# Optimization experiments

Hardware: AMD Instinct MI355X
Metric: run time of the kernel (lower is better)

Reference implementation:

```python
import jax, jax.numpy as jnp
import numpy as np
from math import erf, pi, sqrt, exp

D = 2048
TARGET_BITS = 2.5
N_HIGH = 1024  # round(D * frac)
N_LOW = D - N_HIGH
HIGH_MSE_BITS = 2  # ceil(2.5) - 1
LOW_MSE_BITS = 1   # floor(2.5) - 1


def _phi(x):
    return np.exp(-0.5 * x * x) / np.sqrt(2.0 * np.pi)


def _Phi(x):
    return 0.5 * (1.0 + np.vectorize(erf)(x / np.sqrt(2.0)))


def lloyd_max_centroids(bits: int) -> np.ndarray:
    """Lloyd-Max optimal scalar quantizer centroids for N(0,1), 2**bits levels."""
    L = 2 ** bits
    c = np.linspace(-2.0, 2.0, L)
    for _ in range(200):
        b = 0.5 * (c[:-1] + c[1:])                      # decision boundaries
        edges = np.concatenate([[-1e9], b, [1e9]])
        lo, hi = edges[:-1], edges[1:]
        mass = _Phi(hi) - _Phi(lo)
        c = (_phi(lo) - _phi(hi)) / np.maximum(mass, 1e-12)  # conditional mean
    return c.astype(np.float32)


def generate_rotation_matrix(d: int, seed: int) -> np.ndarray:
    rng = np.random.default_rng(seed)
    A = rng.standard_normal((d, d)).astype(np.float64)
    Q, R = np.linalg.qr(A)
    Q = Q * np.sign(np.diag(R))[None, :]
    return Q.astype(np.float32)


def setup_inputs() -> dict:
    key = jax.random.key(0)
    kq, kk = jax.random.split(key)
    queries = jax.random.normal(kq, (1024, D), dtype=jnp.float32)
    keys = jax.random.normal(kk, (4096, D), dtype=jnp.float32)
    Pi = jnp.asarray(generate_rotation_matrix(D, seed=42 + 2000))
    high_centroids = jnp.asarray(lloyd_max_centroids(HIGH_MSE_BITS))  # (4,)
    low_centroids = jnp.asarray(lloyd_max_centroids(LOW_MSE_BITS))    # (2,)
    rng = np.random.default_rng(42)
    S_high = jnp.asarray(rng.standard_normal((N_HIGH, N_HIGH)).astype(np.float32))
    rng2 = np.random.default_rng(42 + 1000)
    S_low = jnp.asarray(rng2.standard_normal((N_LOW, N_LOW)).astype(np.float32))
    return {"queries": queries, "keys": keys, "Pi": Pi,
            "high_centroids": high_centroids, "low_centroids": low_centroids,
            "S_high": S_high, "S_low": S_low}


def _quantize_group(y, centroids, S):
    # nearest-centroid scalar quantization per channel
    idx = jnp.argmin(jnp.abs(y[..., None] - centroids), axis=-1)  # (bk, n_ch)
    y_mse = centroids[idx]
    residual = y - y_mse
    residual_norm = jnp.linalg.norm(residual, axis=-1)            # (bk,)
    signs = jnp.sign(residual @ S.T)                              # (bk, m)
    return y_mse, signs, residual_norm


def _ip_group(q_ch, y_mse, signs, residual_norm, S):
    m = S.shape[0]
    term1 = q_ch @ y_mse.T                                        # (bq, bk)
    # QJL estimator: <q, r> ~ sqrt(pi/2)/m * ||r|| * <S q, sign(S r)>
    term2 = (jnp.sqrt(jnp.float32(pi / 2)) / m) * ((q_ch @ S.T) @ signs.T) * residual_norm[None, :]
    return term1 + term2


def reference(queries, keys, Pi, high_centroids, low_centroids, S_high, S_low):
    # ---- quantize keys ----
    vec_norm = jnp.linalg.norm(keys, axis=-1)                     # (bk,)
    k_n = keys / (vec_norm[:, None] + 1e-8)
    y = k_n @ Pi.T
    yh, yl = y[:, :N_HIGH], y[:, N_HIGH:]
    kmse_h, sg_h, rn_h = _quantize_group(yh, high_centroids, S_high)
    kmse_l, sg_l, rn_l = _quantize_group(yl, low_centroids, S_low)
    # ---- inner product estimate ----
    q_rot = queries @ Pi.T
    qh, ql = q_rot[:, :N_HIGH], q_rot[:, N_HIGH:]
    ip = _ip_group(qh, kmse_h, sg_h, rn_h, S_high) + _ip_group(ql, kmse_l, sg_l, rn_l, S_low)
    return ip * vec_norm[None, :]                                 # (bq, bk)
```

## Files before the change

### kernel.cpp

```cpp
#include <hip/hip_runtime.h>
#include <math.h>

#ifndef M_PI
#define M_PI 3.14159265358979323846
#endif

typedef __attribute__((ext_vector_type(8))) __bf16 bf16x8;
typedef __attribute__((ext_vector_type(4))) float f32x4;
typedef __attribute__((ext_vector_type(2))) float f32x2;
typedef __attribute__((ext_vector_type(8))) unsigned short ushort8;
typedef __attribute__((ext_vector_type(4))) unsigned short ushort4v;

__device__ __forceinline__ unsigned short f2bf(float x) {
    unsigned int u = __float_as_uint(x);
    unsigned int r = (u + 0x7FFFu + ((u >> 16) & 1u)) >> 16;
    return (unsigned short)r;
}

#define PKFMA_L(d, a, b) \
    asm("v_pk_fma_f32 %0, %1, %2, %0 op_sel:[0,0,0] op_sel_hi:[0,1,1]" \
        : "+v"(d) : "v"(a), "v"(b))
#define PKFMA_H(d, a, b) \
    asm("v_pk_fma_f32 %0, %1, %2, %0 op_sel:[1,0,0] op_sel_hi:[1,1,1]" \
        : "+v"(d) : "v"(a), "v"(b))

__global__ __launch_bounds__(256)
void norm_np_k(const float* __restrict__ keys,
               float* __restrict__ den,
               float* __restrict__ vnorm)
{
#pragma clang fp contract(off)
    const int tid = threadIdx.x;
    const int row_l = tid >> 4;
    const int blk = tid & 15;
    const int row = blockIdx.x * 16 + row_l;
    const float* a = keys + (size_t)row * 2048 + blk * 128;

    float r0 = a[0]*a[0], r1 = a[1]*a[1], r2 = a[2]*a[2], r3 = a[3]*a[3];
    float r4 = a[4]*a[4], r5 = a[5]*a[5], r6 = a[6]*a[6], r7 = a[7]*a[7];
    for (int i = 8; i < 128; i += 8) {
        r0 += a[i+0]*a[i+0]; r1 += a[i+1]*a[i+1];
        r2 += a[i+2]*a[i+2]; r3 += a[i+3]*a[i+3];
        r4 += a[i+4]*a[i+4]; r5 += a[i+5]*a[i+5];
        r6 += a[i+6]*a[i+6]; r7 += a[i+7]*a[i+7];
    }
    float bsum = ((r0 + r1) + (r2 + r3)) + ((r4 + r5) + (r6 + r7));

    __shared__ float bs[16][16];
    bs[row_l][blk] = bsum;
    __syncthreads();
    if (blk == 0) {
        const float* b = bs[row_l];
        float q0 = ((b[0] + b[1]) + (b[2] + b[3])) + ((b[4] + b[5]) + (b[6] + b[7]));
        float q1 = ((b[8] + b[9]) + (b[10] + b[11])) + ((b[12] + b[13]) + (b[14] + b[15]));
        float s = q0 + q1;
        float n = (float)sqrt((double)s);
        den[row] = n + 1e-8f;
        vnorm[row] = n;
    }
}

__global__ __launch_bounds__(256)
void kn_k(const float* __restrict__ keys,
          const float* __restrict__ den,
          float* __restrict__ kn)
{
#pragma clang fp contract(off)
    const int idx = (blockIdx.x * 256 + threadIdx.x) * 8;
    const int row = idx >> 11;
    const float d = den[row];
    float4 v0 = *(const float4*)(keys + idx);
    float4 v1 = *(const float4*)(keys + idx + 4);
    v0.x /= d; v0.y /= d; v0.z /= d; v0.w /= d;
    v1.x /= d; v1.y /= d; v1.z /= d; v1.w /= d;
    *(float4*)(kn + idx) = v0;
    *(float4*)(kn + idx + 4) = v1;
}

__global__ __launch_bounds__(256)
void f2bf_k(const float* __restrict__ in, unsigned short* __restrict__ out)
{
    const int i = (blockIdx.x * 256 + threadIdx.x) * 8;
    float4 v0 = *(const float4*)(in + i);
    float4 v1 = *(const float4*)(in + i + 4);
    ushort8 o;
    o[0] = f2bf(v0.x); o[1] = f2bf(v0.y); o[2] = f2bf(v0.z); o[3] = f2bf(v0.w);
    o[4] = f2bf(v1.x); o[5] = f2bf(v1.y); o[6] = f2bf(v1.z); o[7] = f2bf(v1.w);
    *(ushort8*)(out + i) = o;
}

template <int EPI>
__global__ __launch_bounds__(256, 2)
void gemm_dec_k(const float* __restrict__ A, int lda, int a_zoff,
                const float* __restrict__ B0, const float* __restrict__ B1,
                int ldb,
                float* __restrict__ Cf, unsigned short* __restrict__ Cb,
                int c_zoff, int ldc, int K,
                const float* __restrict__ rv0, const float* __restrict__ rv1)
{
#pragma clang fp contract(off)
    __shared__ float Bs[2][32][132];

    const int z = blockIdx.z;
    const float* Ap = A + (size_t)z * a_zoff;
    const float* Bp = z ? B1 : B0;
    const float* rvp = z ? rv1 : rv0;
    unsigned short* Cbp = (EPI == 1) ? (Cb + (size_t)z * c_zoff) : nullptr;

    const int tid = threadIdx.x;
    const int tr4 = (tid >> 4) * 4;
    const int tc4 = (tid & 15) * 4;
    const int row0 = blockIdx.y * 128;
    const int col0 = blockIdx.x * 128;
    const int sc  = tid >> 1;
    const int skb = (tid & 1) * 16;

    const float* gb = Bp + (size_t)(col0 + sc) * ldb + skb;

    const float* garow[8];
    #pragma unroll
    for (int i = 0; i < 4; ++i) {
        garow[i]     = Ap + (size_t)(row0 + tr4 + i) * lda;
        garow[4 + i] = Ap + (size_t)(row0 + 64 + tr4 + i) * lda;
    }

    f32x2 acc[8][4] = {};
    f32x2 agA[16], agB[16];
    float sb[16];

#define ALOAD(dst, koff) do { \
    _Pragma("unroll") \
    for (int r = 0; r < 8; ++r) \
        *(float4*)&dst[2 * r] = *(const float4*)(garow[r] + (koff)); \
} while (0)

#define BLOADG(koff) do { \
    *(float4*)(sb)      = *(const float4*)(gb + (koff)); \
    *(float4*)(sb + 4)  = *(const float4*)(gb + (koff) + 4); \
    *(float4*)(sb + 8)  = *(const float4*)(gb + (koff) + 8); \
    *(float4*)(sb + 12) = *(const float4*)(gb + (koff) + 12); \
} while (0)

#define BSTORE(buf) do { \
    _Pragma("unroll") \
    for (int u = 0; u < 16; ++u) Bs[buf][skb + u][sc] = sb[u]; \
} while (0)

    BLOADG(0);
    BSTORE(0);
    ALOAD(agA, 0);
    __syncthreads();
    int cur = 0;

    for (int k0 = 0; k0 < K; k0 += 32) {
        const bool moreP = (k0 + 32 < K);
        if (moreP) BLOADG(k0 + 32);

        #pragma unroll
        for (int g = 0; g < 8; ++g) {
            const int nko = k0 + (g + 1) * 4;
            if ((g & 1) == 0) { if (nko < K) ALOAD(agB, nko); }
            else              { if (nko < K) ALOAD(agA, nko); }
            const f32x2* acur = (g & 1) ? agB : agA;

            #pragma unroll
            for (int j = 0; j < 4; ++j) {
                const int kk = g * 4 + j;
                float4 vb0 = *(const float4*)&Bs[cur][kk][tc4];
                float4 vb1 = *(const float4*)&Bs[cur][kk][tc4 + 64];
                f32x2 fb[4];
                fb[0] = (f32x2){vb0.x, vb0.y}; fb[1] = (f32x2){vb0.z, vb0.w};
                fb[2] = (f32x2){vb1.x, vb1.y}; fb[3] = (f32x2){vb1.z, vb1.w};
                #pragma unroll
                for (int r = 0; r < 8; ++r) {
                    const f32x2 ap = acur[2 * r + (j >> 1)];
                    #pragma unroll
                    for (int q = 0; q < 4; ++q) {
                        if (j & 1) { PKFMA_H(acc[r][q], ap, fb[q]); }
                        else       { PKFMA_L(acc[r][q], ap, fb[q]); }
                    }
                }
            }
        }

        if (moreP) BSTORE(cur ^ 1);
        __syncthreads();
        cur ^= 1;
    }

    #pragma unroll
    for (int r = 0; r < 8; ++r) {
        const int row = row0 + ((r < 4) ? (tr4 + r) : (64 + tr4 + r - 4));
        if (EPI == 0) {
            float4 lo4 = {acc[r][0].x, acc[r][0].y, acc[r][1].x, acc[r][1].y};
            float4 hi4 = {acc[r][2].x, acc[r][2].y, acc[r][3].x, acc[r][3].y};
            *(float4*)&Cf[(size_t)row * ldc + col0 + tc4]      = lo4;
            *(float4*)&Cf[(size_t)row * ldc + col0 + 64 + tc4] = hi4;
        } else {
            const float s = rvp[row];
            float v[8] = {acc[r][0].x, acc[r][0].y, acc[r][1].x, acc[r][1].y,
                          acc[r][2].x, acc[r][2].y, acc[r][3].x, acc[r][3].y};
            ushort4v o0, o1;
            #pragma unroll
            for (int j = 0; j < 4; ++j) {
                const float t0 = v[j];
                o0[j] = f2bf((t0 > 0.0f) ? s : ((t0 < 0.0f) ? -s : 0.0f));
                const float t1 = v[4 + j];
                o1[j] = f2bf((t1 > 0.0f) ? s : ((t1 < 0.0f) ? -s : 0.0f));
            }
            *(ushort4v*)&Cbp[(size_t)row * ldc + col0 + tc4]      = o0;
            *(ushort4v*)&Cbp[(size_t)row * ldc + col0 + 64 + tc4] = o1;
        }
    }
#undef ALOAD
#undef BLOADG
#undef BSTORE
}

__global__ __launch_bounds__(256)
void quant_k(float* __restrict__ Y,
             unsigned short* __restrict__ Bmse,
             const float* __restrict__ ch,
             const float* __restrict__ cl,
             float* __restrict__ sc_h,
             float* __restrict__ sc_l,
             double coefd)
{
#pragma clang fp contract(off)
    const int row = blockIdx.x;
    const int tid = threadIdx.x;
    const int c0 = tid * 8;
    const float h0 = ch[0], h1 = ch[1], h2 = ch[2], h3 = ch[3];
    const float l0 = cl[0], l1 = cl[1];

    float y[8], res[8];
    ushort8 cb;
    *(float4*)(y)     = *(const float4*)(Y + (size_t)row * 2048 + c0);
    *(float4*)(y + 4) = *(const float4*)(Y + (size_t)row * 2048 + c0 + 4);

    const bool high = (tid < 128);
    float ss = 0.0f;
    #pragma unroll
    for (int j = 0; j < 8; ++j) {
        const float v = y[j];
        float cbest;
        if (high) {
            cbest = h0;
            float bd = fabsf(v - h0), dd;
            dd = fabsf(v - h1); if (dd < bd) { bd = dd; cbest = h1; }
            dd = fabsf(v - h2); if (dd < bd) { bd = dd; cbest = h2; }
            dd = fabsf(v - h3); if (dd < bd) { bd = dd; cbest = h3; }
        } else {
            cbest = (fabsf(v - l1) < fabsf(v - l0)) ? l1 : l0;
        }
        res[j] = v - cbest;
        cb[j] = f2bf(cbest);
        ss += res[j] * res[j];
    }
    *(float4*)(Y + (size_t)row * 2048 + c0)     = *(float4*)(res);
    *(float4*)(Y + (size_t)row * 2048 + c0 + 4) = *(float4*)(res + 4);
    *(ushort8*)(Bmse + (size_t)row * 4096 + c0) = cb;

    __shared__ float sm[256];
    sm[tid] = ss;
    __syncthreads();
    for (int o = 64; o > 0; o >>= 1) {
        if ((tid & 127) < o) sm[tid] += sm[tid + o];
        __syncthreads();
    }
    if (tid == 0)   sc_h[row] = (float)(coefd * sqrt((double)sm[0]));
    if (tid == 128) sc_l[row] = (float)(coefd * sqrt((double)sm[128]));
}

template <int EPI>
__global__ __launch_bounds__(256)
void gemm_mfma_k(const unsigned short* __restrict__ A, int lda, int a_zoff,
                 const unsigned short* __restrict__ B0,
                 const unsigned short* __restrict__ B1, int ldb,
                 float* __restrict__ Cf, unsigned short* __restrict__ Cb,
                 int c_zoff, int ldc, int K,
                 const float* __restrict__ colscale)
{
    __shared__ unsigned short As[128][40];
    __shared__ unsigned short Bs[128][40];

    const int z = blockIdx.z;
    const unsigned short* Ap = A + (size_t)z * a_zoff;
    const unsigned short* Bp = z ? B1 : B0;
    unsigned short* Cbp = (EPI == 2) ? (Cb + (size_t)z * c_zoff) : nullptr;

    const int tid = threadIdx.x;
    const int lane = tid & 63;
    const int wid = tid >> 6;
    const int wm = wid >> 1;
    const int wn = wid & 1;
    const int row0 = blockIdx.y * 128;
    const int col0 = blockIdx.x * 128;
    const int sr = tid >> 1;
    const int sk = (tid & 1) * 16;
    const int frow = lane & 15;
    const int fk = (lane >> 4) * 8;

    const unsigned short* ga = Ap + (size_t)(row0 + sr) * lda + sk;
    const unsigned short* gb = Bp + (size_t)(col0 + sr) * ldb + sk;

    f32x4 acc[4][4] = {};

    for (int k0 = 0; k0 < K; k0 += 32) {
        ushort8 a0 = *(const ushort8*)(ga + k0);
        ushort8 a1 = *(const ushort8*)(ga + k0 + 8);
        ushort8 b0 = *(const ushort8*)(gb + k0);
        ushort8 b1 = *(const ushort8*)(gb + k0 + 8);
        __syncthreads();
        *(ushort8*)&As[sr][sk]     = a0;
        *(ushort8*)&As[sr][sk + 8] = a1;
        *(ushort8*)&Bs[sr][sk]     = b0;
        *(ushort8*)&Bs[sr][sk + 8] = b1;
        __syncthreads();

        bf16x8 af[4], bfr[4];
        #pragma unroll
        for (int mi = 0; mi < 4; ++mi)
            af[mi] = *(const bf16x8*)&As[wm * 64 + mi * 16 + frow][fk];
        #pragma unroll
        for (int ni = 0; ni < 4; ++ni)
            bfr[ni] = *(const bf16x8*)&Bs[wn * 64 + ni * 16 + frow][fk];
        #pragma unroll
        for (int mi = 0; mi < 4; ++mi)
            #pragma unroll
            for (int ni = 0; ni < 4; ++ni)
                acc[mi][ni] = __builtin_amdgcn_mfma_f32_16x16x32_bf16(
                    af[mi], bfr[ni], acc[mi][ni], 0, 0, 0);
    }

    const int drow = (lane >> 4) * 4;
    const int dcol = lane & 15;
    #pragma unroll
    for (int mi = 0; mi < 4; ++mi) {
        #pragma unroll
        for (int ni = 0; ni < 4; ++ni) {
            const int c = col0 + wn * 64 + ni * 16 + dcol;
            const float cs = (EPI == 1) ? colscale[c] : 0.0f;
            #pragma unroll
            for (int rg = 0; rg < 4; ++rg) {
                const int r = row0 + wm * 64 + mi * 16 + drow + rg;
                const float v = acc[mi][ni][rg];
                if (EPI == 1) Cf[(size_t)r * ldc + c] = v * cs;
                else          Cbp[(size_t)r * ldc + c] = f2bf(v);
            }
        }
    }
}

extern "C" void kernel_launch(void* const* d_in, const int* in_sizes, int n_in,
                              void* d_out, int out_size, void* d_ws, size_t ws_size,
                              hipStream_t stream)
{
    const float* queries = (const float*)d_in[0];
    const float* keys    = (const float*)d_in[1];
    const float* Pi      = (const float*)d_in[2];
    const float* ch      = (const float*)d_in[3];
    const float* cl      = (const float*)d_in[4];
    const float* S_high  = (const float*)d_in[5];
    const float* S_low   = (const float*)d_in[6];
    float* out = (float*)d_out;

    char* ws = (char*)d_ws;
    float*          kn    = (float*)(ws);
    float*          Y     = (float*)(ws + ((size_t)32 << 20));
    unsigned short* Bbig  = (unsigned short*)(ws + ((size_t)64 << 20));
    unsigned short* Abig  = (unsigned short*)(ws + ((size_t)96 << 20));
    unsigned short* Qb    = (unsigned short*)(ws + ((size_t)104 << 20));
    unsigned short* Pib   = (unsigned short*)(ws + ((size_t)108 << 20));
    unsigned short* Sbh   = (unsigned short*)(ws + ((size_t)116 << 20));
    unsigned short* Sbl   = (unsigned short*)(ws + ((size_t)118 << 20));
    float*          den   = (float*)(ws + ((size_t)120 << 20));
    float*          vnorm = (float*)(ws + ((size_t)120 << 20) + 16384);
    float*          sc_h  = (float*)(ws + ((size_t)120 << 20) + 32768);
    float*          sc_l  = (float*)(ws + ((size_t)120 << 20) + 49152);

    const double coefd = sqrt(M_PI / 2.0) / 1024.0;

    norm_np_k<<<256, 256, 0, stream>>>(keys, den, vnorm);

    kn_k<<<4096, 256, 0, stream>>>(keys, den, kn);

    f2bf_k<<<1024, 256, 0, stream>>>(queries, Qb);
    f2bf_k<<<2048, 256, 0, stream>>>(Pi, Pib);
    f2bf_k<<<512, 256, 0, stream>>>(S_high, Sbh);
    f2bf_k<<<512, 256, 0, stream>>>(S_low, Sbl);

    gemm_dec_k<0><<<dim3(16, 32, 1), 256, 0, stream>>>(
        kn, 2048, 0, Pi, Pi, 2048, Y, nullptr, 0, 2048, 2048, nullptr, nullptr);

    quant_k<<<4096, 256, 0, stream>>>(Y, Bbig, ch, cl, sc_h, sc_l, coefd);

    gemm_dec_k<1><<<dim3(8, 32, 2), 256, 0, stream>>>(
        Y, 2048, 1024, S_high, S_low, 1024,
        nullptr, Bbig + 2048, 1024, 4096, 1024, sc_h, sc_l);

    gemm_mfma_k<2><<<dim3(16, 8, 1), 256, 0, stream>>>(
        Qb, 2048, 0, Pib, Pib, 2048, nullptr, Abig, 0, 4096, 2048, nullptr);
    gemm_mfma_k<2><<<dim3(8, 8, 2), 256, 0, stream>>>(
        Abig, 4096, 1024, Sbh, Sbl, 1024, nullptr, Abig + 2048, 1024, 4096, 1024, nullptr);

    gemm_mfma_k<1><<<dim3(32, 8, 1), 256, 0, stream>>>(
        Abig, 4096, 0, Bbig, Bbig, 4096, out, nullptr, 0, 4096, 4096, vnorm);
}
```

Measured before the change: 864.2 us.

## Stage A tile through LDS and enlarge fp32 GEMM tile to 256 rows

```diff
diff --git a/kernel.cpp b/kernel.cpp
--- a/kernel.cpp
+++ b/kernel.cpp
@@ -99,7 +99,8 @@
                 const float* __restrict__ rv0, const float* __restrict__ rv1)
 {
 #pragma clang fp contract(off)
-    __shared__ float Bs[2][32][132];
+    __shared__ float As[2][256][21];
+    __shared__ float Bs[2][16][132];
 
     const int z = blockIdx.z;
     const float* Ap = A + (size_t)z * a_zoff;
@@ -108,89 +109,89 @@
     unsigned short* Cbp = (EPI == 1) ? (Cb + (size_t)z * c_zoff) : nullptr;
 
     const int tid = threadIdx.x;
-    const int tr4 = (tid >> 4) * 4;
+    const int tr = tid >> 4;
     const int tc4 = (tid & 15) * 4;
-    const int row0 = blockIdx.y * 128;
+    const int row0 = blockIdx.y * 256;
     const int col0 = blockIdx.x * 128;
-    const int sc  = tid >> 1;
-    const int skb = (tid & 1) * 16;
-
-    const float* gb = Bp + (size_t)(col0 + sc) * ldb + skb;
-
-    const float* garow[8];
-    #pragma unroll
-    for (int i = 0; i < 4; ++i) {
-        garow[i]     = Ap + (size_t)(row0 + tr4 + i) * lda;
-        garow[4 + i] = Ap + (size_t)(row0 + 64 + tr4 + i) * lda;
-    }
-
-    f32x2 acc[8][4] = {};
-    f32x2 agA[16], agB[16];
-    float sb[16];
-
-#define ALOAD(dst, koff) do { \
+
+    const int arow = tid >> 2;
+    const int akf  = (tid & 3) * 4;
+    const int bcol = tid >> 1;
+    const int bk   = (tid & 1) * 8;
+
+    const float* gb = Bp + (size_t)(col0 + bcol) * ldb + bk;
+
+    f32x2 acc[16][4] = {};
+    float4 sa[4];
+    float4 sbv0, sbv1;
+
+#define LOADSTAGE(koff) do { \
     _Pragma("unroll") \
-    for (int r = 0; r < 8; ++r) \
-        *(float4*)&dst[2 * r] = *(const float4*)(garow[r] + (koff)); \
+    for (int j4 = 0; j4 < 4; ++j4) \
+        sa[j4] = *(const float4*)(Ap + (size_t)(row0 + arow + j4 * 64) * lda + (koff) + akf); \
+    sbv0 = *(const float4*)(gb + (koff)); \
+    sbv1 = *(const float4*)(gb + (koff) + 4); \
 } while (0)
 
-#define BLOADG(koff) do { \
-    *(float4*)(sb)      = *(const float4*)(gb + (koff)); \
-    *(float4*)(sb + 4)  = *(const float4*)(gb + (koff) + 4); \
-    *(float4*)(sb + 8)  = *(const float4*)(gb + (koff) + 8); \
-    *(float4*)(sb + 12) = *(const float4*)(gb + (koff) + 12); \
+#define STORESTAGE(buf) do { \
+    _Pragma("unroll") \
+    for (int j4 = 0; j4 < 4; ++j4) \
+        *(float4*)&As[buf][arow + j4 * 64][akf] = sa[j4]; \
+    Bs[buf][bk + 0][bcol] = sbv0.x; Bs[buf][bk + 1][bcol] = sbv0.y; \
+    Bs[buf][bk + 2][bcol] = sbv0.z; Bs[buf][bk + 3][bcol] = sbv0.w; \
+    Bs[buf][bk + 4][bcol] = sbv1.x; Bs[buf][bk + 5][bcol] = sbv1.y; \
+    Bs[buf][bk + 6][bcol] = sbv1.z; Bs[buf][bk + 7][bcol] = sbv1.w; \
 } while (0)
 
-#define BSTORE(buf) do { \
-    _Pragma("unroll") \
-    for (int u = 0; u < 16; ++u) Bs[buf][skb + u][sc] = sb[u]; \
-} while (0)
-
-    BLOADG(0);
-    BSTORE(0);
-    ALOAD(agA, 0);
+    LOADSTAGE(0);
+    STORESTAGE(0);
     __syncthreads();
     int cur = 0;
 
-    for (int k0 = 0; k0 < K; k0 += 32) {
-        const bool moreP = (k0 + 32 < K);
-        if (moreP) BLOADG(k0 + 32);
+    for (int k0 = 0; k0 < K; k0 += 16) {
+        const bool more = (k0 + 16 < K);
+        if (more) LOADSTAGE(k0 + 16);
 
         #pragma unroll
-        for (int g = 0; g < 8; ++g) {
-            const int nko = k0 + (g + 1) * 4;
-            if ((g & 1) == 0) { if (nko < K) ALOAD(agB, nko); }
-            else              { if (nko < K) ALOAD(agA, nko); }
-            const f32x2* acur = (g & 1) ? agB : agA;
-
+        for (int g = 0; g < 4; ++g) {
+            f32x2 fb[4][4];
             #pragma unroll
             for (int j = 0; j < 4; ++j) {
-                const int kk = g * 4 + j;
-                float4 vb0 = *(const float4*)&Bs[cur][kk][tc4];
-                float4 vb1 = *(const float4*)&Bs[cur][kk][tc4 + 64];
-                f32x2 fb[4];
-                fb[0] = (f32x2){vb0.x, vb0.y}; fb[1] = (f32x2){vb0.z, vb0.w};
-                fb[2] = (f32x2){vb1.x, vb1.y}; fb[3] = (f32x2){vb1.z, vb1.w};
+                float4 vb0 = *(const float4*)&Bs[cur][g * 4 + j][tc4];
+                float4 vb1 = *(const float4*)&Bs[cur][g * 4 + j][tc4 + 64];
+                fb[j][0] = (f32x2){vb0.x, vb0.y};
+                fb[j][1] = (f32x2){vb0.z, vb0.w};
+                fb[j][2] = (f32x2){vb1.x, vb1.y};
+                fb[j][3] = (f32x2){vb1.z, vb1.w};
+            }
+            #pragma unroll
+            for (int m = 0; m < 4; ++m) {
                 #pragma unroll
-                for (int r = 0; r < 8; ++r) {
-                    const f32x2 ap = acur[2 * r + (j >> 1)];
+                for (int i = 0; i < 4; ++i) {
+                    float4 a4 = *(const float4*)&As[cur][m * 64 + tr * 4 + i][g * 4];
+                    f32x2 a01 = (f32x2){a4.x, a4.y};
+                    f32x2 a23 = (f32x2){a4.z, a4.w};
+                    const int r = m * 4 + i;
                     #pragma unroll
-                    for (int q = 0; q < 4; ++q) {
-                        if (j & 1) { PKFMA_H(acc[r][q], ap, fb[q]); }
-                        else       { PKFMA_L(acc[r][q], ap, fb[q]); }
-                    }
+                    for (int q = 0; q < 4; ++q) PKFMA_L(acc[r][q], a01, fb[0][q]);
+                    #pragma unroll
+                    for (int q = 0; q < 4; ++q) PKFMA_H(acc[r][q], a01, fb[1][q]);
+                    #pragma unroll
+                    for (int q = 0; q < 4; ++q) PKFMA_L(acc[r][q], a23, fb[2][q]);
+                    #pragma unroll
+                    for (int q = 0; q < 4; ++q) PKFMA_H(acc[r][q], a23, fb[3][q]);
                 }
             }
         }
 
-        if (moreP) BSTORE(cur ^ 1);
+        if (more) STORESTAGE(cur ^ 1);
         __syncthreads();
         cur ^= 1;
     }
 
     #pragma unroll
-    for (int r = 0; r < 8; ++r) {
-        const int row = row0 + ((r < 4) ? (tr4 + r) : (64 + tr4 + r - 4));
+    for (int r = 0; r < 16; ++r) {
+        const int row = row0 + (r >> 2) * 64 + tr * 4 + (r & 3);
         if (EPI == 0) {
             float4 lo4 = {acc[r][0].x, acc[r][0].y, acc[r][1].x, acc[r][1].y};
             float4 hi4 = {acc[r][2].x, acc[r][2].y, acc[r][3].x, acc[r][3].y};
@@ -212,9 +213,8 @@
             *(ushort4v*)&Cbp[(size_t)row * ldc + col0 + 64 + tc4] = o1;
         }
     }
-#undef ALOAD
-#undef BLOADG
-#undef BSTORE
+#undef LOADSTAGE
+#undef STORESTAGE
 }
 
 __global__ __launch_bounds__(256)
@@ -390,12 +390,12 @@
     f2bf_k<<<512, 256, 0, stream>>>(S_high, Sbh);
     f2bf_k<<<512, 256, 0, stream>>>(S_low, Sbl);
 
-    gemm_dec_k<0><<<dim3(16, 32, 1), 256, 0, stream>>>(
+    gemm_dec_k<0><<<dim3(16, 16, 1), 256, 0, stream>>>(
         kn, 2048, 0, Pi, Pi, 2048, Y, nullptr, 0, 2048, 2048, nullptr, nullptr);
 
     quant_k<<<4096, 256, 0, stream>>>(Y, Bbig, ch, cl, sc_h, sc_l, coefd);
 
-    gemm_dec_k<1><<<dim3(8, 32, 2), 256, 0, stream>>>(
+    gemm_dec_k<1><<<dim3(8, 16, 2), 256, 0, stream>>>(
         Y, 2048, 1024, S_high, S_low, 1024,
         nullptr, Bbig + 2048, 1024, 4096, 1024, sc_h, sc_l);
 
```

Measured after the change: 1.206 ms. +39.5%, slower.
